# Kernel optimization log

Hardware: AMD Instinct MI355X
Metric: run time of the kernel (lower is better)

The kernel has to match this reference:

```python
import jax, jax.numpy as jnp
import numpy as np

DIM = 128
NUM_HEADS = 4
WIN = (7, 7)
N = WIN[0] * WIN[1]
HEAD_DIM = DIM // NUM_HEADS
SCALE = HEAD_DIM ** -0.5
NW = 64


def _relative_position_index():
    coords_h = np.arange(WIN[0])
    coords_w = np.arange(WIN[1])
    coords = np.stack(np.meshgrid(coords_h, coords_w, indexing='ij'))  # [2, Wh, Ww]
    cf = coords.reshape(2, -1)
    rel = cf[:, :, None] - cf[:, None, :]  # [2, N, N]
    rel = rel.transpose(1, 2, 0)
    rel[:, :, 0] += WIN[0] - 1
    rel[:, :, 1] += WIN[1] - 1
    rel[:, :, 0] *= 2 * WIN[1] - 1
    return rel.sum(-1).astype(np.int32)  # [N, N]


def setup_inputs() -> dict:
    key = jax.random.key(0)
    ks = jax.random.split(key, 8)
    B_ = 4096  # num_windows_per_image * image_batch = 64 * 64
    x = jax.random.normal(ks[0], (B_, N, DIM), dtype=jnp.float32)
    mask = jax.random.normal(ks[1], (NW, N, N), dtype=jnp.float32)  # additive shift mask
    qkv_w = jax.random.normal(ks[2], (DIM, 3 * DIM), dtype=jnp.float32) * (DIM ** -0.5)
    qkv_b = jnp.zeros((3 * DIM,), dtype=jnp.float32)
    proj_w = jax.random.normal(ks[3], (DIM, DIM), dtype=jnp.float32) * (DIM ** -0.5)
    proj_b = jnp.zeros((DIM,), dtype=jnp.float32)
    rel_bias_table = jax.random.normal(ks[4], ((2 * WIN[0] - 1) * (2 * WIN[1] - 1), NUM_HEADS), dtype=jnp.float32) * 0.02
    rel_index = jnp.asarray(_relative_position_index())
    return {"x": x, "mask": mask, "qkv_w": qkv_w, "qkv_b": qkv_b,
            "proj_w": proj_w, "proj_b": proj_b,
            "rel_bias_table": rel_bias_table, "rel_index": rel_index}


def reference(x, mask, qkv_w, qkv_b, proj_w, proj_b, rel_bias_table, rel_index):
    B_, n, C = x.shape
    # qkv projection -> [3, B_, H, N, hd]
    qkv = (x @ qkv_w + qkv_b).reshape(B_, n, 3, NUM_HEADS, HEAD_DIM)
    qkv = jnp.transpose(qkv, (2, 0, 3, 1, 4))
    q, k, v = qkv[0], qkv[1], qkv[2]
    attn = jnp.einsum('bhnd,bhmd->bhnm', q * SCALE, k)  # [B_, H, N, N]
    # gathered relative position bias: [N, N, H] -> [H, N, N]
    bias = rel_bias_table[rel_index.reshape(-1)].reshape(n, n, NUM_HEADS)
    attn = attn + jnp.transpose(bias, (2, 0, 1))[None]
    # additive shift mask, broadcast over image batch
    nW = mask.shape[0]
    attn = attn.reshape(-1, nW, NUM_HEADS, n, n) + mask[None, :, None]
    attn = attn.reshape(-1, NUM_HEADS, n, n)
    attn = jax.nn.softmax(attn, axis=-1)
    out = jnp.einsum('bhnm,bhmd->bnhd', attn, v).reshape(B_, n, C)
    return out @ proj_w + proj_b
```

## Files before the change

kernel.cpp:

```cpp
#include <hip/hip_runtime.h>

#define NWIN 49
#define DIM  128
#define NH   4
#define HD   32
#define SCALE 0.17677669529663687f

using short8 = __attribute__((ext_vector_type(8))) short;
using f32x4  = __attribute__((ext_vector_type(4))) float;

union Frag { uint4 u; short8 s; };

static __device__ __forceinline__ short8 ld8(const unsigned short* p) {
    Frag fr; fr.u = *(const uint4*)p; return fr.s;
}
static __device__ __forceinline__ unsigned short f2bf(float f) {
    union { float f; unsigned i; } v; v.f = f;
    unsigned r = v.i + 0x7fffu + ((v.i >> 16) & 1u);
    return (unsigned short)(r >> 16);
}

__global__ __launch_bounds__(256) void prep_kernel(
    const float* __restrict__ qkv_w,
    const float* __restrict__ proj_w,
    const float* __restrict__ mask,
    const float* __restrict__ bias_tab,
    const int*   __restrict__ rel_index,
    unsigned short* __restrict__ wqkvT,
    unsigned short* __restrict__ projT,
    float*          __restrict__ BM)
{
    int tid = blockIdx.x * 256 + threadIdx.x;
    if (tid < 49152) {
        int n = tid >> 7, k = tid & 127;
        wqkvT[tid] = f2bf(qkv_w[k * 384 + n]);
    } else if (tid < 65536) {
        int t2 = tid - 49152;
        int n = t2 >> 7, k = t2 & 127;
        projT[t2] = f2bf(proj_w[k * 128 + n]);
    } else if (tid < 65536 + 64 * NH * 2401) {
        int idx = tid - 65536;
        int wh = idx / 2401, ij = idx % 2401;
        int wm = wh >> 2, h = wh & 3;
        BM[idx] = mask[wm * 2401 + ij] + bias_tab[rel_index[ij] * NH + h];
    }
}

#define XS_STRIDE 136
#define WPOOL_OFF 13328
#define WPOOL_SZ  12448
#define QH_OFF    4608
#define KH_OFF    8528
#define PS_OFF    4608
#define POOL_SZ   65168

__global__ __launch_bounds__(256) void winattn_kernel(
    const float* __restrict__ x,
    const float* __restrict__ qkv_b,
    const float* __restrict__ proj_b,
    const unsigned short* __restrict__ wqkvT,
    const unsigned short* __restrict__ projT,
    const float* __restrict__ BM,
    float*       __restrict__ out)
{
    __shared__ __align__(16) char pool[POOL_SZ];
    unsigned short* XS = (unsigned short*)pool;

    const int b = blockIdx.x;
    const int t = threadIdx.x;
    const int w = t >> 6;
    const int lane = t & 63;
    const int q = lane >> 4;
    const int l16 = lane & 15;
    const int wm = b & 63;
    const int h = w;

    char* wp = pool + WPOOL_OFF + w * WPOOL_SZ;
    unsigned short* VT = (unsigned short*)wp;
    unsigned short* QH = (unsigned short*)(wp + QH_OFF);
    unsigned short* KH = (unsigned short*)(wp + KH_OFF);
    unsigned short* PS = (unsigned short*)(wp + PS_OFF);

    for (int c = t; c < NWIN * 16; c += 256) {
        const int row = c >> 4, g = c & 15;
        const float4* src = (const float4*)(x + (size_t)b * (NWIN * DIM) + row * DIM + g * 8);
        float4 f0 = src[0], f1 = src[1];
        uint4 p;
        p.x = (unsigned)f2bf(f0.x) | ((unsigned)f2bf(f0.y) << 16);
        p.y = (unsigned)f2bf(f0.z) | ((unsigned)f2bf(f0.w) << 16);
        p.z = (unsigned)f2bf(f1.x) | ((unsigned)f2bf(f1.y) << 16);
        p.w = (unsigned)f2bf(f1.z) | ((unsigned)f2bf(f1.w) << 16);
        *(uint4*)(XS + row * XS_STRIDE + g * 8) = p;
    }
    __syncthreads();

    #pragma unroll
    for (int job = 0; job < 24; ++job) {
        const int mt = job & 3, sn = job >> 2, s = sn >> 1, nn = sn & 1;
        const int colbase = s * 128 + h * 32 + nn * 16;
        f32x4 acc = {0.f, 0.f, 0.f, 0.f};
        const unsigned short* arow = XS + (mt * 16 + l16) * XS_STRIDE + q * 8;
        const unsigned short* brow = wqkvT + (size_t)(colbase + l16) * 128 + q * 8;
        #pragma unroll
        for (int ks = 0; ks < 4; ++ks)
            acc = __builtin_amdgcn_mfma_f32_16x16x32_bf16(ld8(arow + ks * 32),
                                                          ld8(brow + ks * 32), acc, 0, 0, 0);
        const float bias = qkv_b[colbase + l16];
        const int cl = nn * 16 + l16;
        #pragma unroll
        for (int r = 0; r < 4; ++r) {
            const int row = mt * 16 + q * 4 + r;
            const float val = acc[r] + bias;
            if (s == 0)      { if (row < NWIN) QH[row * 40 + cl] = f2bf(val * SCALE); }
            else if (s == 1) { if (row < NWIN) KH[row * 40 + cl] = f2bf(val); }
            else             VT[cl * 72 + row] = f2bf(val);
        }
    }
    __syncthreads();

    float sv[4][4][4];
    {
        short8 bfr[4];
        #pragma unroll
        for (int nt = 0; nt < 4; ++nt)
            bfr[nt] = ld8(KH + (nt * 16 + l16) * 40 + q * 8);
        #pragma unroll
        for (int mt = 0; mt < 4; ++mt) {
            short8 a = ld8(QH + (mt * 16 + l16) * 40 + q * 8);
            #pragma unroll
            for (int nt = 0; nt < 4; ++nt) {
                f32x4 acc = {0.f, 0.f, 0.f, 0.f};
                acc = __builtin_amdgcn_mfma_f32_16x16x32_bf16(a, bfr[nt], acc, 0, 0, 0);
                #pragma unroll
                for (int r = 0; r < 4; ++r) sv[mt][nt][r] = acc[r];
            }
        }
    }
    {
        const float* bm = BM + (size_t)(wm * NH + h) * 2401;
        #pragma unroll
        for (int mt = 0; mt < 4; ++mt)
            #pragma unroll
            for (int r = 0; r < 4; ++r) {
                const int i = mt * 16 + q * 4 + r;
                const float* bmr = bm + i * 49;
                #pragma unroll
                for (int nt = 0; nt < 4; ++nt) {
                    const int j = nt * 16 + l16;
                    if (j >= NWIN)      sv[mt][nt][r] = -1e30f;
                    else if (i < NWIN)  sv[mt][nt][r] += bmr[j];
                }
            }
    }
    #pragma unroll
    for (int mt = 0; mt < 4; ++mt)
        #pragma unroll
        for (int r = 0; r < 4; ++r) {
            float m = fmaxf(fmaxf(sv[mt][0][r], sv[mt][1][r]),
                            fmaxf(sv[mt][2][r], sv[mt][3][r]));
            m = fmaxf(m, __shfl_xor(m, 1));
            m = fmaxf(m, __shfl_xor(m, 2));
            m = fmaxf(m, __shfl_xor(m, 4));
            m = fmaxf(m, __shfl_xor(m, 8));
            float sum = 0.f;
            #pragma unroll
            for (int nt = 0; nt < 4; ++nt) {
                float e = __expf(sv[mt][nt][r] - m);
                sv[mt][nt][r] = e;
                sum += e;
            }
            sum += __shfl_xor(sum, 1);
            sum += __shfl_xor(sum, 2);
            sum += __shfl_xor(sum, 4);
            sum += __shfl_xor(sum, 8);
            const float rs = 1.f / sum;
            const int i = mt * 16 + q * 4 + r;
            if (i < NWIN) {
                #pragma unroll
                for (int nt = 0; nt < 4; ++nt)
                    PS[i * 72 + nt * 16 + l16] = f2bf(sv[mt][nt][r] * rs);
            }
        }

    #pragma unroll
    for (int nt2 = 0; nt2 < 2; ++nt2) {
        short8 bv0 = ld8(VT + (nt2 * 16 + l16) * 72 + q * 8);
        short8 bv1 = ld8(VT + (nt2 * 16 + l16) * 72 + 32 + q * 8);
        #pragma unroll
        for (int mt = 0; mt < 4; ++mt) {
            f32x4 acc = {0.f, 0.f, 0.f, 0.f};
            acc = __builtin_amdgcn_mfma_f32_16x16x32_bf16(
                ld8(PS + (mt * 16 + l16) * 72 + q * 8), bv0, acc, 0, 0, 0);
            acc = __builtin_amdgcn_mfma_f32_16x16x32_bf16(
                ld8(PS + (mt * 16 + l16) * 72 + 32 + q * 8), bv1, acc, 0, 0, 0);
            #pragma unroll
            for (int r = 0; r < 4; ++r) {
                const int row = mt * 16 + q * 4 + r;
                if (row < NWIN)
                    XS[row * XS_STRIDE + h * 32 + nt2 * 16 + l16] = f2bf(acc[r]);
            }
        }
    }
    __syncthreads();

    for (int job = w; job < 32; job += 4) {
        const int mt = job >> 3, nt = job & 7;
        f32x4 acc = {0.f, 0.f, 0.f, 0.f};
        const unsigned short* arow = XS + (mt * 16 + l16) * XS_STRIDE + q * 8;
        const unsigned short* brow = projT + (size_t)(nt * 16 + l16) * 128 + q * 8;
        #pragma unroll
        for (int ks = 0; ks < 4; ++ks)
            acc = __builtin_amdgcn_mfma_f32_16x16x32_bf16(ld8(arow + ks * 32),
                                                          ld8(brow + ks * 32), acc, 0, 0, 0);
        const int col = nt * 16 + l16;
        const float pb = proj_b[col];
        #pragma unroll
        for (int r = 0; r < 4; ++r) {
            const int row = mt * 16 + q * 4 + r;
            if (row < NWIN)
                out[(size_t)b * (NWIN * DIM) + row * 128 + col] = acc[r] + pb;
        }
    }
}

extern "C" void kernel_launch(void* const* d_in, const int* in_sizes, int n_in,
                              void* d_out, int out_size, void* d_ws, size_t ws_size,
                              hipStream_t stream) {
    const int B = in_sizes[0] / (NWIN * DIM);
    unsigned short* wqkvT = (unsigned short*)d_ws;
    unsigned short* projT = (unsigned short*)((char*)d_ws + 98304);
    float*          BM    = (float*)((char*)d_ws + 131072);

    prep_kernel<<<2657, 256, 0, stream>>>(
        (const float*)d_in[2],
        (const float*)d_in[4],
        (const float*)d_in[1],
        (const float*)d_in[6],
        (const int*)d_in[7],
        wqkvT, projT, BM);

    winattn_kernel<<<B, 256, 0, stream>>>(
        (const float*)d_in[0],
        (const float*)d_in[3],
        (const float*)d_in[5],
        wqkvT, projT, BM,
        (float*)d_out);
}
```

Baseline: 357.1 us.

## Split fused window attention into chunked QKV and attention kernels

Replaces the single fused window-attention kernel with two kernels run over chunks of windows: one computes bf16 Q (pre-scaled), K and transposed V into workspace, the other does scores, bias/mask, softmax, PV and the output projection. Chunk size is derived from workspace size, and the old fused kernel remains as a fallback. The intent is to cut per-block LDS use and raise occupancy in each stage, at the cost of extra global-memory round trips for Q/K/V and more kernel launches.

```diff
diff --git a/kernel.cpp b/kernel.cpp
--- a/kernel.cpp
+++ b/kernel.cpp
@@ -7,6 +7,7 @@
 #define SCALE 0.17677669529663687f
 
 using short8 = __attribute__((ext_vector_type(8))) short;
+using us4    = __attribute__((ext_vector_type(4))) unsigned short;
 using f32x4  = __attribute__((ext_vector_type(4))) float;
 
 union Frag { uint4 u; short8 s; };
@@ -46,6 +47,211 @@
     }
 }
 
+__global__ __launch_bounds__(256) void qkv_kernel(
+    const float* __restrict__ x,
+    const float* __restrict__ qkv_b,
+    const unsigned short* __restrict__ wqkvT,
+    unsigned short* __restrict__ Qb,
+    unsigned short* __restrict__ Kb,
+    unsigned short* __restrict__ VT,
+    int c0, int Mtot)
+{
+    __shared__ __align__(16) unsigned short XS[64 * 136];
+    const int lb = blockIdx.x, t = threadIdx.x;
+    const int w = t >> 6, lane = t & 63, q = lane >> 4, l16 = lane & 15;
+
+    for (int c = t; c < 64 * 16; c += 256) {
+        const int row = c >> 4, g = c & 15;
+        int grow = (c0 + lb) * NWIN + row;
+        if (grow > Mtot - 1) grow = Mtot - 1;
+        const float4* src = (const float4*)(x + (size_t)grow * DIM + g * 8);
+        float4 f0 = src[0], f1 = src[1];
+        uint4 p;
+        p.x = (unsigned)f2bf(f0.x) | ((unsigned)f2bf(f0.y) << 16);
+        p.y = (unsigned)f2bf(f0.z) | ((unsigned)f2bf(f0.w) << 16);
+        p.z = (unsigned)f2bf(f1.x) | ((unsigned)f2bf(f1.y) << 16);
+        p.w = (unsigned)f2bf(f1.z) | ((unsigned)f2bf(f1.w) << 16);
+        *(uint4*)(XS + row * 136 + g * 8) = p;
+    }
+    __syncthreads();
+
+    short8 af[4][4];
+    #pragma unroll
+    for (int mt = 0; mt < 4; ++mt)
+        #pragma unroll
+        for (int ks = 0; ks < 4; ++ks)
+            af[mt][ks] = ld8(XS + (mt * 16 + l16) * 136 + ks * 32 + q * 8);
+
+    #pragma unroll
+    for (int sn = 0; sn < 6; ++sn) {
+        const int s = sn >> 1, nn = sn & 1;
+        const int colbase = s * 128 + w * 32 + nn * 16;
+        short8 bfr[4];
+        #pragma unroll
+        for (int ks = 0; ks < 4; ++ks)
+            bfr[ks] = ld8(wqkvT + (size_t)(colbase + l16) * 128 + ks * 32 + q * 8);
+        const float bias = qkv_b[colbase + l16];
+        const int cl = nn * 16 + l16;
+        #pragma unroll
+        for (int mt = 0; mt < 4; ++mt) {
+            f32x4 acc = {0.f, 0.f, 0.f, 0.f};
+            #pragma unroll
+            for (int ks = 0; ks < 4; ++ks)
+                acc = __builtin_amdgcn_mfma_f32_16x16x32_bf16(af[mt][ks], bfr[ks], acc, 0, 0, 0);
+            if (s == 2) {
+                us4 pk;
+                #pragma unroll
+                for (int r = 0; r < 4; ++r) pk[r] = f2bf(acc[r] + bias);
+                *(us4*)(VT + ((size_t)(lb * 4 + w) * 32 + cl) * 64 + mt * 16 + q * 4) = pk;
+            } else {
+                #pragma unroll
+                for (int r = 0; r < 4; ++r) {
+                    const int row = mt * 16 + q * 4 + r;
+                    if (row < NWIN) {
+                        const float val = acc[r] + bias;
+                        if (s == 0)
+                            Qb[(size_t)(lb * NWIN + row) * 128 + w * 32 + cl] = f2bf(val * SCALE);
+                        else
+                            Kb[(size_t)(lb * NWIN + row) * 128 + w * 32 + cl] = f2bf(val);
+                    }
+                }
+            }
+        }
+    }
+}
+
+#define PSS 72
+#define OSS 136
+#define OS_BYTES  (NWIN * OSS * 2)
+#define PSW_BYTES (64 * PSS * 2)
+
+__global__ __launch_bounds__(256) void attn_kernel(
+    const unsigned short* __restrict__ Qb,
+    const unsigned short* __restrict__ Kb,
+    const unsigned short* __restrict__ VT,
+    const float* __restrict__ BM,
+    const unsigned short* __restrict__ projT,
+    const float* __restrict__ proj_b,
+    float* __restrict__ out,
+    int c0)
+{
+    __shared__ __align__(16) char pool[OS_BYTES + 4 * PSW_BYTES];
+    unsigned short* OS = (unsigned short*)pool;
+
+    const int lb = blockIdx.x, t = threadIdx.x;
+    const int w = t >> 6, lane = t & 63, q = lane >> 4, l16 = lane & 15;
+    const int h = w, wm = (c0 + lb) & 63;
+    unsigned short* PS = (unsigned short*)(pool + OS_BYTES + w * PSW_BYTES);
+
+    const unsigned short* qb = Qb + (size_t)lb * NWIN * 128 + h * 32 + q * 8;
+    const unsigned short* kb = Kb + (size_t)lb * NWIN * 128 + h * 32 + q * 8;
+
+    float sv[4][4][4];
+    {
+        short8 kf[4];
+        #pragma unroll
+        for (int nt = 0; nt < 4; ++nt)
+            kf[nt] = ld8(kb + (nt * 16 + l16) * 128);
+        #pragma unroll
+        for (int mt = 0; mt < 4; ++mt) {
+            short8 a = ld8(qb + (mt * 16 + l16) * 128);
+            #pragma unroll
+            for (int nt = 0; nt < 4; ++nt) {
+                f32x4 acc = {0.f, 0.f, 0.f, 0.f};
+                acc = __builtin_amdgcn_mfma_f32_16x16x32_bf16(a, kf[nt], acc, 0, 0, 0);
+                #pragma unroll
+                for (int r = 0; r < 4; ++r) sv[mt][nt][r] = acc[r];
+            }
+        }
+    }
+    {
+        const float* bm = BM + (size_t)(wm * NH + h) * 2401;
+        #pragma unroll
+        for (int mt = 0; mt < 4; ++mt)
+            #pragma unroll
+            for (int r = 0; r < 4; ++r) {
+                const int i = mt * 16 + q * 4 + r;
+                const float* bmr = bm + i * 49;
+                #pragma unroll
+                for (int nt = 0; nt < 4; ++nt) {
+                    const int j = nt * 16 + l16;
+                    if (j >= NWIN)      sv[mt][nt][r] = -1e30f;
+                    else if (i < NWIN)  sv[mt][nt][r] += bmr[j];
+                }
+            }
+    }
+    #pragma unroll
+    for (int mt = 0; mt < 4; ++mt)
+        #pragma unroll
+        for (int r = 0; r < 4; ++r) {
+            float m = fmaxf(fmaxf(sv[mt][0][r], sv[mt][1][r]),
+                            fmaxf(sv[mt][2][r], sv[mt][3][r]));
+            m = fmaxf(m, __shfl_xor(m, 1));
+            m = fmaxf(m, __shfl_xor(m, 2));
+            m = fmaxf(m, __shfl_xor(m, 4));
+            m = fmaxf(m, __shfl_xor(m, 8));
+            float sum = 0.f;
+            #pragma unroll
+            for (int nt = 0; nt < 4; ++nt) {
+                float e = __expf(sv[mt][nt][r] - m);
+                sv[mt][nt][r] = e;
+                sum += e;
+            }
+            sum += __shfl_xor(sum, 1);
+            sum += __shfl_xor(sum, 2);
+            sum += __shfl_xor(sum, 4);
+            sum += __shfl_xor(sum, 8);
+            const float rs = 1.f / sum;
+            const int i = mt * 16 + q * 4 + r;
+            if (i < NWIN) {
+                #pragma unroll
+                for (int nt = 0; nt < 4; ++nt)
+                    PS[i * PSS + nt * 16 + l16] = f2bf(sv[mt][nt][r] * rs);
+            }
+        }
+
+    const unsigned short* vb = VT + (size_t)(lb * 4 + h) * 32 * 64;
+    #pragma unroll
+    for (int nt2 = 0; nt2 < 2; ++nt2) {
+        short8 bv0 = ld8(vb + (nt2 * 16 + l16) * 64 + q * 8);
+        short8 bv1 = ld8(vb + (nt2 * 16 + l16) * 64 + 32 + q * 8);
+        #pragma unroll
+        for (int mt = 0; mt < 4; ++mt) {
+            f32x4 acc = {0.f, 0.f, 0.f, 0.f};
+            acc = __builtin_amdgcn_mfma_f32_16x16x32_bf16(
+                ld8(PS + (mt * 16 + l16) * PSS + q * 8), bv0, acc, 0, 0, 0);
+            acc = __builtin_amdgcn_mfma_f32_16x16x32_bf16(
+                ld8(PS + (mt * 16 + l16) * PSS + 32 + q * 8), bv1, acc, 0, 0, 0);
+            #pragma unroll
+            for (int r = 0; r < 4; ++r) {
+                const int row = mt * 16 + q * 4 + r;
+                if (row < NWIN)
+                    OS[row * OSS + h * 32 + nt2 * 16 + l16] = f2bf(acc[r]);
+            }
+        }
+    }
+    __syncthreads();
+
+    for (int job = w; job < 32; job += 4) {
+        const int mt = job >> 3, nt = job & 7;
+        f32x4 acc = {0.f, 0.f, 0.f, 0.f};
+        const unsigned short* arow = OS + (mt * 16 + l16) * OSS + q * 8;
+        const unsigned short* brow = projT + (size_t)(nt * 16 + l16) * 128 + q * 8;
+        #pragma unroll
+        for (int ks = 0; ks < 4; ++ks)
+            acc = __builtin_amdgcn_mfma_f32_16x16x32_bf16(ld8(arow + ks * 32),
+                                                          ld8(brow + ks * 32), acc, 0, 0, 0);
+        const int col = nt * 16 + l16;
+        const float pb = proj_b[col];
+        #pragma unroll
+        for (int r = 0; r < 4; ++r) {
+            const int row = mt * 16 + q * 4 + r;
+            if (row < NWIN)
+                out[(size_t)lb * (NWIN * DIM) + row * 128 + col] = acc[r] + pb;
+        }
+    }
+}
+
 #define XS_STRIDE 136
 #define WPOOL_OFF 13328
 #define WPOOL_SZ  12448
@@ -227,9 +433,11 @@
                               void* d_out, int out_size, void* d_ws, size_t ws_size,
                               hipStream_t stream) {
     const int B = in_sizes[0] / (NWIN * DIM);
+    const int M = B * NWIN;
     unsigned short* wqkvT = (unsigned short*)d_ws;
     unsigned short* projT = (unsigned short*)((char*)d_ws + 98304);
     float*          BM    = (float*)((char*)d_ws + 131072);
+    const size_t FIXED = 131072 + 2458624;
 
     prep_kernel<<<2657, 256, 0, stream>>>(
         (const float*)d_in[2],
@@ -239,10 +447,36 @@
         (const int*)d_in[7],
         wqkvT, projT, BM);
 
-    winattn_kernel<<<B, 256, 0, stream>>>(
-        (const float*)d_in[0],
-        (const float*)d_in[3],
-        (const float*)d_in[5],
-        wqkvT, projT, BM,
-        (float*)d_out);
-}
+    size_t CW = 0;
+    if (ws_size > FIXED + 32768) {
+        size_t avail = ws_size - FIXED;
+        CW = (avail - 32768) / 41472;
+        if (CW > (size_t)B) CW = (size_t)B;
+    }
+
+    if (CW >= 32) {
+        char* pbase = (char*)d_ws + FIXED;
+        const size_t qk_bytes = ((size_t)CW * NWIN + 64) * 256;
+        unsigned short* Qb  = (unsigned short*)pbase;
+        unsigned short* Kb  = (unsigned short*)(pbase + qk_bytes);
+        unsigned short* VTb = (unsigned short*)(pbase + 2 * qk_bytes);
+        for (int c0 = 0; c0 < B; c0 += (int)CW) {
+            int cw = (B - c0) < (int)CW ? (B - c0) : (int)CW;
+            qkv_kernel<<<cw, 256, 0, stream>>>(
+                (const float*)d_in[0],
+                (const float*)d_in[3],
+                wqkvT, Qb, Kb, VTb, c0, M);
+            attn_kernel<<<cw, 256, 0, stream>>>(
+                Qb, Kb, VTb, BM, projT,
+                (const float*)d_in[5],
+                (float*)d_out + (size_t)c0 * NWIN * DIM, c0);
+        }
+    } else {
+        winattn_kernel<<<B, 256, 0, stream>>>(
+            (const float*)d_in[0],
+            (const float*)d_in[3],
+            (const float*)d_in[5],
+            wqkvT, projT, BM,
+            (float*)d_out);
+    }
+}
```

Result: slower. 401.7 us (+12.5%).

## Double block size to 512 threads and split row tiles across warp pairs

Applied to the files above, without the earlier changes.

Launches 8 warps per window instead of 4. QKV projection, attention and output projection work is split so two warps share each head by row tiles, and projection warps each own one column tile. A/B fragments are hoisted into registers for reuse across tiles. An extra barrier is added before writing the probability tile, because it aliases Q/K storage now read by two warps. This raises waves per CU under the same shared-memory footprint, at the cost of an additional block-wide sync.

```diff
diff --git a/kernel.cpp b/kernel.cpp
--- a/kernel.cpp
+++ b/kernel.cpp
@@ -54,7 +54,7 @@
 #define PS_OFF    4608
 #define POOL_SZ   65168
 
-__global__ __launch_bounds__(256) void winattn_kernel(
+__global__ __launch_bounds__(512) void winattn_kernel(
     const float* __restrict__ x,
     const float* __restrict__ qkv_b,
     const float* __restrict__ proj_b,
@@ -73,15 +73,8 @@
     const int q = lane >> 4;
     const int l16 = lane & 15;
     const int wm = b & 63;
-    const int h = w;
-
-    char* wp = pool + WPOOL_OFF + w * WPOOL_SZ;
-    unsigned short* VT = (unsigned short*)wp;
-    unsigned short* QH = (unsigned short*)(wp + QH_OFF);
-    unsigned short* KH = (unsigned short*)(wp + KH_OFF);
-    unsigned short* PS = (unsigned short*)(wp + PS_OFF);
-
-    for (int c = t; c < NWIN * 16; c += 256) {
+
+    for (int c = t; c < NWIN * 16; c += 512) {
         const int row = c >> 4, g = c & 15;
         const float4* src = (const float4*)(x + (size_t)b * (NWIN * DIM) + row * DIM + g * 8);
         float4 f0 = src[0], f1 = src[1];
@@ -94,70 +87,100 @@
     }
     __syncthreads();
 
-    #pragma unroll
-    for (int job = 0; job < 24; ++job) {
-        const int mt = job & 3, sn = job >> 2, s = sn >> 1, nn = sn & 1;
-        const int colbase = s * 128 + h * 32 + nn * 16;
-        f32x4 acc = {0.f, 0.f, 0.f, 0.f};
-        const unsigned short* arow = XS + (mt * 16 + l16) * XS_STRIDE + q * 8;
-        const unsigned short* brow = wqkvT + (size_t)(colbase + l16) * 128 + q * 8;
-        #pragma unroll
-        for (int ks = 0; ks < 4; ++ks)
-            acc = __builtin_amdgcn_mfma_f32_16x16x32_bf16(ld8(arow + ks * 32),
-                                                          ld8(brow + ks * 32), acc, 0, 0, 0);
-        const float bias = qkv_b[colbase + l16];
-        const int cl = nn * 16 + l16;
-        #pragma unroll
-        for (int r = 0; r < 4; ++r) {
-            const int row = mt * 16 + q * 4 + r;
-            const float val = acc[r] + bias;
-            if (s == 0)      { if (row < NWIN) QH[row * 40 + cl] = f2bf(val * SCALE); }
-            else if (s == 1) { if (row < NWIN) KH[row * 40 + cl] = f2bf(val); }
-            else             VT[cl * 72 + row] = f2bf(val);
-        }
-    }
-    __syncthreads();
-
-    float sv[4][4][4];
-    {
-        short8 bfr[4];
+    {
+        const int hb = w & 3;
+        const int mt0 = w >> 2;
+        char* wpb = pool + WPOOL_OFF + hb * WPOOL_SZ;
+        unsigned short* VTb = (unsigned short*)wpb;
+        unsigned short* QHb = (unsigned short*)(wpb + QH_OFF);
+        unsigned short* KHb = (unsigned short*)(wpb + KH_OFF);
+
+        short8 af[2][4];
+        #pragma unroll
+        for (int mti = 0; mti < 2; ++mti) {
+            const int mt = mt0 + 2 * mti;
+            #pragma unroll
+            for (int ks = 0; ks < 4; ++ks)
+                af[mti][ks] = ld8(XS + (mt * 16 + l16) * XS_STRIDE + ks * 32 + q * 8);
+        }
+        #pragma unroll
+        for (int sn = 0; sn < 6; ++sn) {
+            const int s = sn >> 1, nn = sn & 1;
+            const int colbase = s * 128 + hb * 32 + nn * 16;
+            short8 bfr[4];
+            #pragma unroll
+            for (int ks = 0; ks < 4; ++ks)
+                bfr[ks] = ld8(wqkvT + (size_t)(colbase + l16) * 128 + ks * 32 + q * 8);
+            const float bias = qkv_b[colbase + l16];
+            const int cl = nn * 16 + l16;
+            #pragma unroll
+            for (int mti = 0; mti < 2; ++mti) {
+                const int mt = mt0 + 2 * mti;
+                f32x4 acc = {0.f, 0.f, 0.f, 0.f};
+                #pragma unroll
+                for (int ks = 0; ks < 4; ++ks)
+                    acc = __builtin_amdgcn_mfma_f32_16x16x32_bf16(af[mti][ks], bfr[ks], acc, 0, 0, 0);
+                #pragma unroll
+                for (int r = 0; r < 4; ++r) {
+                    const int row = mt * 16 + q * 4 + r;
+                    const float val = acc[r] + bias;
+                    if (s == 0)      { if (row < NWIN) QHb[row * 40 + cl] = f2bf(val * SCALE); }
+                    else if (s == 1) { if (row < NWIN) KHb[row * 40 + cl] = f2bf(val); }
+                    else             VTb[cl * 72 + row] = f2bf(val);
+                }
+            }
+        }
+    }
+    __syncthreads();
+
+    const int h = w >> 1, mh = w & 1;
+    char* wp = pool + WPOOL_OFF + h * WPOOL_SZ;
+    unsigned short* VT = (unsigned short*)wp;
+    unsigned short* QH = (unsigned short*)(wp + QH_OFF);
+    unsigned short* KH = (unsigned short*)(wp + KH_OFF);
+    unsigned short* PS = (unsigned short*)(wp + PS_OFF);
+
+    float sv[2][4][4];
+    {
+        short8 kf[4];
         #pragma unroll
         for (int nt = 0; nt < 4; ++nt)
-            bfr[nt] = ld8(KH + (nt * 16 + l16) * 40 + q * 8);
-        #pragma unroll
-        for (int mt = 0; mt < 4; ++mt) {
+            kf[nt] = ld8(KH + (nt * 16 + l16) * 40 + q * 8);
+        #pragma unroll
+        for (int mti = 0; mti < 2; ++mti) {
+            const int mt = 2 * mh + mti;
             short8 a = ld8(QH + (mt * 16 + l16) * 40 + q * 8);
             #pragma unroll
             for (int nt = 0; nt < 4; ++nt) {
                 f32x4 acc = {0.f, 0.f, 0.f, 0.f};
-                acc = __builtin_amdgcn_mfma_f32_16x16x32_bf16(a, bfr[nt], acc, 0, 0, 0);
-                #pragma unroll
-                for (int r = 0; r < 4; ++r) sv[mt][nt][r] = acc[r];
+                acc = __builtin_amdgcn_mfma_f32_16x16x32_bf16(a, kf[nt], acc, 0, 0, 0);
+                #pragma unroll
+                for (int r = 0; r < 4; ++r) sv[mti][nt][r] = acc[r];
             }
         }
     }
     {
         const float* bm = BM + (size_t)(wm * NH + h) * 2401;
         #pragma unroll
-        for (int mt = 0; mt < 4; ++mt)
+        for (int mti = 0; mti < 2; ++mti)
             #pragma unroll
             for (int r = 0; r < 4; ++r) {
-                const int i = mt * 16 + q * 4 + r;
+                const int i = (2 * mh + mti) * 16 + q * 4 + r;
                 const float* bmr = bm + i * 49;
                 #pragma unroll
                 for (int nt = 0; nt < 4; ++nt) {
                     const int j = nt * 16 + l16;
-                    if (j >= NWIN)      sv[mt][nt][r] = -1e30f;
-                    else if (i < NWIN)  sv[mt][nt][r] += bmr[j];
+                    if (j >= NWIN)      sv[mti][nt][r] = -1e30f;
+                    else if (i < NWIN)  sv[mti][nt][r] += bmr[j];
                 }
             }
     }
     #pragma unroll
-    for (int mt = 0; mt < 4; ++mt)
+    for (int mti = 0; mti < 2; ++mti)
         #pragma unroll
         for (int r = 0; r < 4; ++r) {
-            float m = fmaxf(fmaxf(sv[mt][0][r], sv[mt][1][r]),
-                            fmaxf(sv[mt][2][r], sv[mt][3][r]));
+            float m = fmaxf(fmaxf(sv[mti][0][r], sv[mti][1][r]),
+                            fmaxf(sv[mti][2][r], sv[mti][3][r]));
             m = fmaxf(m, __shfl_xor(m, 1));
             m = fmaxf(m, __shfl_xor(m, 2));
             m = fmaxf(m, __shfl_xor(m, 4));
@@ -165,8 +188,8 @@
             float sum = 0.f;
             #pragma unroll
             for (int nt = 0; nt < 4; ++nt) {
-                float e = __expf(sv[mt][nt][r] - m);
-                sv[mt][nt][r] = e;
+                float e = __expf(sv[mti][nt][r] - m);
+                sv[mti][nt][r] = e;
                 sum += e;
             }
             sum += __shfl_xor(sum, 1);
@@ -174,11 +197,21 @@
             sum += __shfl_xor(sum, 4);
             sum += __shfl_xor(sum, 8);
             const float rs = 1.f / sum;
-            const int i = mt * 16 + q * 4 + r;
+            #pragma unroll
+            for (int nt = 0; nt < 4; ++nt) sv[mti][nt][r] *= rs;
+        }
+
+    __syncthreads();
+
+    #pragma unroll
+    for (int mti = 0; mti < 2; ++mti)
+        #pragma unroll
+        for (int r = 0; r < 4; ++r) {
+            const int i = (2 * mh + mti) * 16 + q * 4 + r;
             if (i < NWIN) {
                 #pragma unroll
                 for (int nt = 0; nt < 4; ++nt)
-                    PS[i * 72 + nt * 16 + l16] = f2bf(sv[mt][nt][r] * rs);
+                    PS[i * 72 + nt * 16 + l16] = f2bf(sv[mti][nt][r]);
             }
         }
 
@@ -187,7 +220,8 @@
         short8 bv0 = ld8(VT + (nt2 * 16 + l16) * 72 + q * 8);
         short8 bv1 = ld8(VT + (nt2 * 16 + l16) * 72 + 32 + q * 8);
         #pragma unroll
-        for (int mt = 0; mt < 4; ++mt) {
+        for (int mti = 0; mti < 2; ++mti) {
+            const int mt = 2 * mh + mti;
             f32x4 acc = {0.f, 0.f, 0.f, 0.f};
             acc = __builtin_amdgcn_mfma_f32_16x16x32_bf16(
                 ld8(PS + (mt * 16 + l16) * 72 + q * 8), bv0, acc, 0, 0, 0);
@@ -203,22 +237,28 @@
     }
     __syncthreads();
 
-    for (int job = w; job < 32; job += 4) {
-        const int mt = job >> 3, nt = job & 7;
-        f32x4 acc = {0.f, 0.f, 0.f, 0.f};
-        const unsigned short* arow = XS + (mt * 16 + l16) * XS_STRIDE + q * 8;
-        const unsigned short* brow = projT + (size_t)(nt * 16 + l16) * 128 + q * 8;
+    {
+        const int nt = w;
+        short8 bfr[4];
         #pragma unroll
         for (int ks = 0; ks < 4; ++ks)
-            acc = __builtin_amdgcn_mfma_f32_16x16x32_bf16(ld8(arow + ks * 32),
-                                                          ld8(brow + ks * 32), acc, 0, 0, 0);
+            bfr[ks] = ld8(projT + (size_t)(nt * 16 + l16) * 128 + ks * 32 + q * 8);
         const int col = nt * 16 + l16;
         const float pb = proj_b[col];
         #pragma unroll
-        for (int r = 0; r < 4; ++r) {
-            const int row = mt * 16 + q * 4 + r;
-            if (row < NWIN)
-                out[(size_t)b * (NWIN * DIM) + row * 128 + col] = acc[r] + pb;
+        for (int mt = 0; mt < 4; ++mt) {
+            f32x4 acc = {0.f, 0.f, 0.f, 0.f};
+            const unsigned short* arow = XS + (mt * 16 + l16) * XS_STRIDE + q * 8;
+            #pragma unroll
+            for (int ks = 0; ks < 4; ++ks)
+                acc = __builtin_amdgcn_mfma_f32_16x16x32_bf16(ld8(arow + ks * 32),
+                                                              bfr[ks], acc, 0, 0, 0);
+            #pragma unroll
+            for (int r = 0; r < 4; ++r) {
+                const int row = mt * 16 + q * 4 + r;
+                if (row < NWIN)
+                    out[(size_t)b * (NWIN * DIM) + row * 128 + col] = acc[r] + pb;
+            }
         }
     }
 }
@@ -239,7 +279,7 @@
         (const int*)d_in[7],
         wqkvT, projT, BM);
 
-    winattn_kernel<<<B, 256, 0, stream>>>(
+    winattn_kernel<<<B, 512, 0, stream>>>(
         (const float*)d_in[0],
         (const float*)d_in[3],
         (const float*)d_in[5],
```

Result: faster. 327.4 us (-8.3%).
